# Optimization experiments

Hardware: AMD Instinct MI355X
Metric: run time of the kernel (lower is better)

## Reference

```python
import jax, jax.numpy as jnp
import numpy as np

ITERATIONS = 20  # Resonator(iterations=20)
B, F, V, D = 128, 4, 2048, 4096


def _hardsign(x):
    # bipolar normalization used by MAP-VSA multiset(normalize=True); ties -> +1
    return jnp.where(x >= 0, 1.0, -1.0).astype(x.dtype)


def setup_inputs() -> dict:
    key = jax.random.key(0)
    k1, k2 = jax.random.split(key, 2)
    # bipolar codebooks: (F, V, D)
    codebooks = _hardsign(jax.random.normal(k1, (F, V, D), dtype=jnp.float32))
    # a realistic composite input: bind (elementwise product) of one codevector per factor
    idx = jax.random.randint(k2, (B, F), 0, V)                       # (B, F)
    chosen = codebooks[jnp.arange(F)[None, :], idx]                  # (B, F, D)
    inputs = jnp.prod(chosen, axis=1)                                # (B, D)
    # standard resonator init: normalized superposition of each codebook
    init_estimates = jnp.broadcast_to(
        _hardsign(jnp.sum(codebooks, axis=1)), (B, F, D)
    ).astype(jnp.float32)                                            # (B, F, D)
    return {"inputs": inputs, "init_estimates": init_estimates, "codebooks": codebooks}


def _resonator_step(inputs, est, codebooks):
    # est: (B, F, D). rolled stack over k=1..F-1 -> (B, F, F-1, D)
    f = est.shape[-2]
    rolled = jnp.stack([jnp.roll(est, k, axis=-2) for k in range(1, f)], axis=-2)
    inv_others = jnp.prod(rolled, axis=-2)          # multibind over dim -2 -> (B, F, D)
    new_est = inputs[:, None, :] * inv_others       # bind -> (B, F, D)
    sim = jnp.einsum('bfd,fvd->bfv', new_est, codebooks)   # similarity (activation='NONE')
    # multiset(codebooks, sim, normalize=True)
    return _hardsign(jnp.einsum('bfv,fvd->bfd', sim, codebooks))


def reference(inputs, init_estimates, codebooks):
    def body(carry, i):
        est, k, done = carry
        new = _resonator_step(inputs, est, codebooks)
        eq = jnp.all(new == est)          # convergence check (fixed point)
        k = jnp.where(done, k, i)
        return (new, k, done | eq), None

    carry0 = (init_estimates, jnp.int32(0), jnp.bool_(False))
    (est, k, _), _ = jax.lax.scan(body, carry0, jnp.arange(ITERATIONS, dtype=jnp.int32))
    # cleanup: argmax of |similarity| per factor (argmax_abs=True)
    sim = jnp.einsum('bfd,fvd->bfv', est, codebooks)
    outcome = jnp.argmax(jnp.abs(sim), axis=-1)     # (B, F) int indices
    return outcome, k
```

## Files before the change

kernel.cpp:

```cpp
#include <hip/hip_runtime.h>
#include <hip/hip_bf16.h>
#include <stdint.h>

#define B_    128
#define F_    4
#define V_    2048
#define D_    4096
#define DW    64
#define VW    32
#define ITERS 20
#define NKT   16

typedef _Float16 half8 __attribute__((ext_vector_type(8)));
typedef float   floatx4 __attribute__((ext_vector_type(4)));

__global__ __launch_bounds__(256) void k_pack(const float* __restrict__ x,
                                              uint64_t* __restrict__ bits, int n) {
    int t = blockIdx.x * blockDim.x + threadIdx.x;
    if (t * 16 >= n) return;
    const float4* p = (const float4*)x + (size_t)t * 4;
    uint32_t m = 0;
    #pragma unroll
    for (int j = 0; j < 4; ++j) {
        float4 v = p[j];
        m |= (__float_as_uint(v.x) >> 31) << (4 * j + 0);
        m |= (__float_as_uint(v.y) >> 31) << (4 * j + 1);
        m |= (__float_as_uint(v.z) >> 31) << (4 * j + 2);
        m |= (__float_as_uint(v.w) >> 31) << (4 * j + 3);
    }
    ((unsigned short*)bits)[t] = (unsigned short)m;
}

__global__ void k_packT(const uint64_t* __restrict__ cb_bits,
                        uint64_t* __restrict__ cbT) {
    int vw = blockIdx.x, dwg = blockIdx.y, f = blockIdx.z;
    int lane = threadIdx.x & 63;
    int dw = dwg * 4 + (threadIdx.x >> 6);
    uint64_t w = cb_bits[((size_t)f * V_ + vw * 64 + lane) * DW + dw];
    uint64_t r = 0;
    for (int d2 = 0; d2 < 64; ++d2) {
        uint64_t m = __ballot((unsigned)((w >> d2) & 1));
        if (lane == d2) r = m;
    }
    cbT[((size_t)f * D_ + dw * 64 + lane) * VW + vw] = r;
}

__global__ __launch_bounds__(256) void k_sim(
        const uint64_t* __restrict__ cb_bits,
        const uint64_t* __restrict__ in_bits,
        const uint64_t* __restrict__ est_bits,
        _Float16* __restrict__ simf,
        const int* __restrict__ flags, int iter) {
    if (iter > 0 && flags[iter - 1] == 0) return;
    int vt = blockIdx.x, bt = blockIdx.y, f = blockIdx.z;
    int v0 = vt * 64, b0 = bt * 64;
    int tid = threadIdx.x;

    __shared__ __align__(16) ulonglong2 CB2[64 * 32];
    __shared__ __align__(16) ulonglong2 NB2[64 * 32];

    #pragma unroll
    for (int it = 0; it < 8; ++it) {
        int cq = it * 256 + tid;
        int r = cq >> 5, ch = cq & 31;
        const ulonglong2* src = (const ulonglong2*)(cb_bits + ((size_t)f * V_ + v0 + r) * DW);
        CB2[r * 32 + (ch ^ (r & 7))] = src[ch];
    }
    #pragma unroll
    for (int it = 0; it < 8; ++it) {
        int cq = it * 256 + tid;
        int r = cq >> 5, ch = cq & 31;
        int b = b0 + r;
        const ulonglong2* iv = (const ulonglong2*)(in_bits + (size_t)b * DW);
        const uint64_t* eb = est_bits + (size_t)b * F_ * DW;
        ulonglong2 i2 = iv[ch];
        ulonglong2 e0 = ((const ulonglong2*)(eb + 0 * DW))[ch];
        ulonglong2 e1 = ((const ulonglong2*)(eb + 1 * DW))[ch];
        ulonglong2 e2 = ((const ulonglong2*)(eb + 2 * DW))[ch];
        ulonglong2 e3 = ((const ulonglong2*)(eb + 3 * DW))[ch];
        ulonglong2 es = e0;
        if (f == 1) es = e1; else if (f == 2) es = e2; else if (f == 3) es = e3;
        ulonglong2 val;
        val.x = i2.x ^ e0.x ^ e1.x ^ e2.x ^ e3.x ^ es.x;
        val.y = i2.y ^ e0.y ^ e1.y ^ e2.y ^ e3.y ^ es.y;
        NB2[r * 32 + (ch ^ (r & 7))] = val;
    }
    __syncthreads();

    int vv = tid & 15, bb = tid >> 4;
    int svz = vv & 7, sbz = bb & 7;
    int pc[4][4];
    #pragma unroll
    for (int j = 0; j < 4; ++j)
        #pragma unroll
        for (int i = 0; i < 4; ++i) pc[j][i] = 0;

    #pragma unroll 4
    for (int ch = 0; ch < 32; ++ch) {
        ulonglong2 c[4], n[4];
        #pragma unroll
        for (int i = 0; i < 4; ++i)
            c[i] = CB2[(vv + 16 * i) * 32 + (ch ^ svz)];
        #pragma unroll
        for (int j = 0; j < 4; ++j)
            n[j] = NB2[(bb + 16 * j) * 32 + (ch ^ sbz)];
        #pragma unroll
        for (int j = 0; j < 4; ++j)
            #pragma unroll
            for (int i = 0; i < 4; ++i)
                pc[j][i] += __popcll(n[j].x ^ c[i].x) + __popcll(n[j].y ^ c[i].y);
    }

    #pragma unroll
    for (int j = 0; j < 4; ++j) {
        int b = b0 + bb + 16 * j;
        #pragma unroll
        for (int i = 0; i < 4; ++i) {
            int v = v0 + vv + 16 * i;
            simf[((size_t)f * B_ + b) * V_ + v] = (_Float16)(2048 - pc[j][i]);
        }
    }
}

__global__ __launch_bounds__(256) void k_gemm(
        const _Float16* __restrict__ simf,
        const uint64_t* __restrict__ cbT,
        uint64_t* __restrict__ est_bits,
        int* __restrict__ flags, int iter) {
    if (iter > 0 && flags[iter - 1] == 0) return;
    int nt = blockIdx.x, mt = blockIdx.y, f = blockIdx.z;
    int m0 = mt * 64, n0 = nt * 64;
    int tid = threadIdx.x;
    int lane = tid & 63, wave = tid >> 6;
    int lrow = lane & 15, lq = lane >> 4;
    int wm = wave & 1, wn = wave >> 1;

    __shared__ __align__(16) uint64_t Bb[64 * VW];
    __shared__ __align__(16) _Float16 As[64 * 128];
    __shared__ int bd;
    if (tid == 0) bd = 0;

    const uint64_t* bsrc = cbT + ((size_t)f * D_ + n0) * VW;
    #pragma unroll
    for (int p = 0; p < 4; ++p) {
        int chunk = p * 256 + tid;
        int dloc = chunk >> 4, cw = chunk & 15;
        ulonglong2 val = *(const ulonglong2*)&bsrc[dloc * VW + cw * 2];
        *(ulonglong2*)&Bb[dloc * VW + ((cw ^ (dloc & 15)) * 2)] = val;
    }

    const _Float16* Ab = simf + (size_t)f * B_ * V_ + (size_t)m0 * V_;
    int arow = tid >> 4, acol = tid & 15;
    half8 areg[4];
    #pragma unroll
    for (int p = 0; p < 4; ++p)
        areg[p] = *(const half8*)&Ab[(size_t)(p * 16 + arow) * V_ + acol * 8];

    floatx4 acc[2][2] = {};

    const uint64_t SPREAD = 0x1000200040008000ull;
    const uint64_t SMASK  = 0x8000800080008000ull;
    const uint64_t PONE   = 0x3C003C003C003C00ull;

    #pragma unroll 1
    for (int kt = 0; kt < NKT; ++kt) {
        __syncthreads();
        #pragma unroll
        for (int p = 0; p < 4; ++p)
            *(half8*)&As[(p * 16 + arow) * 128 + ((acol ^ arow) * 8)] = areg[p];
        if (kt + 1 < NKT) {
            #pragma unroll
            for (int p = 0; p < 4; ++p)
                areg[p] = *(const half8*)&Ab[(size_t)(p * 16 + arow) * V_ + (kt + 1) * 128 + acol * 8];
        }
        __syncthreads();

        ulonglong2 bw[2];
        #pragma unroll
        for (int nt2 = 0; nt2 < 2; ++nt2) {
            int dloc = wn * 32 + nt2 * 16 + lrow;
            bw[nt2] = *(const ulonglong2*)&Bb[dloc * VW + ((kt ^ (dloc & 15)) * 2)];
        }
        #pragma unroll
        for (int ks = 0; ks < 4; ++ks) {
            half8 af[2];
            #pragma unroll
            for (int mt2 = 0; mt2 < 2; ++mt2) {
                int row = wm * 32 + mt2 * 16 + lrow;
                af[mt2] = *(const half8*)&As[row * 128 + (((ks * 4 + lq) ^ lrow) * 8)];
            }
            half8 bfrag[2];
            #pragma unroll
            for (int nt2 = 0; nt2 < 2; ++nt2) {
                uint64_t w = (ks < 2) ? bw[nt2].x : bw[nt2].y;
                uint32_t byte = (uint32_t)(w >> ((((ks & 1) * 4 + lq)) * 8)) & 0xFFu;
                union { uint64_t q[2]; half8 h; } bu;
                bu.q[0] = (((uint64_t)(byte & 0xFu) * SPREAD) & SMASK) ^ PONE;
                bu.q[1] = (((uint64_t)(byte >> 4)   * SPREAD) & SMASK) ^ PONE;
                bfrag[nt2] = bu.h;
            }
            #pragma unroll
            for (int mt2 = 0; mt2 < 2; ++mt2)
                #pragma unroll
                for (int nt2 = 0; nt2 < 2; ++nt2)
                    acc[mt2][nt2] = __builtin_amdgcn_mfma_f32_16x16x32_f16(
                        af[mt2], bfrag[nt2], acc[mt2][nt2], 0, 0, 0);
        }
    }

    __syncthreads();
    unsigned char* S = (unsigned char*)As;
    #pragma unroll
    for (int mt2 = 0; mt2 < 2; ++mt2)
        #pragma unroll
        for (int nt2 = 0; nt2 < 2; ++nt2)
            #pragma unroll
            for (int r = 0; r < 4; ++r) {
                int row = wm * 32 + mt2 * 16 + lq * 4 + r;
                int col = wn * 32 + nt2 * 16 + lrow;
                S[row * 64 + col] = (acc[mt2][nt2][r] < 0.0f) ? 1 : 0;
            }
    __syncthreads();
    if (tid < 64) {
        const uint64_t* Sw = (const uint64_t*)S;
        uint64_t m = 0;
        #pragma unroll
        for (int j = 0; j < 8; ++j) {
            uint64_t w = Sw[tid * 8 + j];
            m |= ((w * 0x0102040810204080ull) >> 56) << (8 * j);
        }
        size_t widx = ((size_t)(m0 + tid) * F_ + f) * DW + nt;
        uint64_t old = est_bits[widx];
        est_bits[widx] = m;
        if (old != m) atomicOr(&bd, 1);
    }
    __syncthreads();
    if (tid == 0 && bd) atomicOr(&flags[iter], 1);
}

__global__ __launch_bounds__(256) void k_argmax(
        const uint64_t* __restrict__ cb_bits,
        const uint64_t* __restrict__ est_bits,
        int* __restrict__ keys) {
    int vt = blockIdx.x, f = blockIdx.y;
    int v0 = vt * 32;
    int tid = threadIdx.x;

    __shared__ __align__(16) ulonglong2 EB2[128 * 32];
    __shared__ __align__(16) ulonglong2 CBa[32 * 32];

    #pragma unroll
    for (int it = 0; it < 16; ++it) {
        int cq = it * 256 + tid;
        int r = cq >> 5, ch = cq & 31;
        const ulonglong2* src = (const ulonglong2*)(est_bits + ((size_t)r * F_ + f) * DW);
        EB2[r * 32 + (ch ^ (r & 7))] = src[ch];
    }
    #pragma unroll
    for (int it = 0; it < 4; ++it) {
        int cq = it * 256 + tid;
        int r = cq >> 5, ch = cq & 31;
        const ulonglong2* src = (const ulonglong2*)(cb_bits + ((size_t)f * V_ + v0 + r) * DW);
        CBa[r * 32 + (ch ^ (r & 7))] = src[ch];
    }
    __syncthreads();

    int vv = tid & 15, bb = tid >> 4;
    int svz = vv & 7, sbz = bb & 7;
    int pc[8][2];
    #pragma unroll
    for (int j = 0; j < 8; ++j) { pc[j][0] = 0; pc[j][1] = 0; }

    #pragma unroll 4
    for (int ch = 0; ch < 32; ++ch) {
        ulonglong2 c[2], n[8];
        #pragma unroll
        for (int i = 0; i < 2; ++i)
            c[i] = CBa[(vv + 16 * i) * 32 + (ch ^ svz)];
        #pragma unroll
        for (int j = 0; j < 8; ++j)
            n[j] = EB2[(bb + 16 * j) * 32 + (ch ^ sbz)];
        #pragma unroll
        for (int j = 0; j < 8; ++j)
            #pragma unroll
            for (int i = 0; i < 2; ++i)
                pc[j][i] += __popcll(n[j].x ^ c[i].x) + __popcll(n[j].y ^ c[i].y);
    }

    #pragma unroll
    for (int j = 0; j < 8; ++j) {
        int kj = 0x80000000;
        #pragma unroll
        for (int i = 0; i < 2; ++i) {
            int v = v0 + vv + 16 * i;
            int m = 2048 - pc[j][i]; if (m < 0) m = -m;
            int key = (m << 11) | (2047 - v);
            if (key > kj) kj = key;
        }
        #pragma unroll
        for (int s = 1; s < 16; s <<= 1) {
            int o = __shfl_xor(kj, s, 64);
            if (o > kj) kj = o;
        }
        if ((tid & 15) == 0)
            atomicMax(&keys[(size_t)(bb + 16 * j) * F_ + f], kj);
    }
}

__global__ void k_final(const int* __restrict__ keys, const int* __restrict__ flags,
                        int* __restrict__ out) {
    int tid = blockIdx.x * blockDim.x + threadIdx.x;
    if (tid < B_ * F_) out[tid] = 2047 - (keys[tid] & 0x7FF);
    if (tid == 0) {
        int k = ITERS - 1;
        for (int i = 0; i < ITERS; ++i) if (flags[i] == 0) { k = i; break; }
        out[B_ * F_] = k;
    }
}

extern "C" void kernel_launch(void* const* d_in, const int* in_sizes, int n_in,
                              void* d_out, int out_size, void* d_ws, size_t ws_size,
                              hipStream_t stream) {
    const float* inputs = (const float*)d_in[0];
    const float* inite  = (const float*)d_in[1];
    const float* cb     = (const float*)d_in[2];
    int* out = (int*)d_out;

    char* ws = (char*)d_ws;
    uint64_t* cb_bits  = (uint64_t*)ws;  ws += (size_t)F_ * V_ * DW * 8;
    uint64_t* cbT_bits = (uint64_t*)ws;  ws += (size_t)F_ * D_ * VW * 8;
    uint64_t* est_bits = (uint64_t*)ws;  ws += (size_t)B_ * F_ * DW * 8;
    uint64_t* in_bits  = (uint64_t*)ws;  ws += (size_t)B_ * DW * 8;
    _Float16* simf     = (_Float16*)ws;  ws += (size_t)F_ * B_ * V_ * 2;
    int*      flags    = (int*)ws;       ws += 32 * 4;
    int*      keys     = (int*)ws;       ws += B_ * F_ * 4;

    hipMemsetAsync(flags, 0, (32 + B_ * F_) * sizeof(int), stream);
    k_pack<<<(F_ * V_ * D_) / 4096, 256, 0, stream>>>(cb,     cb_bits,  F_ * V_ * D_);
    k_pack<<<(B_ * F_ * D_) / 4096, 256, 0, stream>>>(inite,  est_bits, B_ * F_ * D_);
    k_pack<<<(B_ * D_) / 4096,      256, 0, stream>>>(inputs, in_bits,  B_ * D_);
    k_packT<<<dim3(32, 16, 4), 256, 0, stream>>>(cb_bits, cbT_bits);

    for (int i = 0; i < ITERS; ++i) {
        k_sim<<<dim3(32, 2, 4), 256, 0, stream>>>(cb_bits, in_bits, est_bits, simf, flags, i);
        k_gemm<<<dim3(64, 2, 4), 256, 0, stream>>>(simf, cbT_bits, est_bits, flags, i);
    }
    k_argmax<<<dim3(64, 4), 256, 0, stream>>>(cb_bits, est_bits, keys);
    k_final<<<2, 256, 0, stream>>>(keys, flags, out);
}
```

Before: 1.005 ms.

## Fuse setup packing and memset into one kernel; halve k_sim batch tile

Merges the three bit-packing launches and the flags/keys memset into a single k_setup kernel. This cuts launch overhead and the memset call. It also halves k_sim's batch tile from 64 to 32 rows, doubling the grid to 512 blocks for better occupancy on the many CUs, at the cost of reloading the codebook tile twice as often. The per-factor estimate select becomes an indexed load.

```diff
diff --git a/kernel.cpp b/kernel.cpp
--- a/kernel.cpp
+++ b/kernel.cpp
@@ -1,5 +1,4 @@
 #include <hip/hip_runtime.h>
-#include <hip/hip_bf16.h>
 #include <stdint.h>
 
 #define B_    128
@@ -14,10 +13,8 @@
 typedef _Float16 half8 __attribute__((ext_vector_type(8)));
 typedef float   floatx4 __attribute__((ext_vector_type(4)));
 
-__global__ __launch_bounds__(256) void k_pack(const float* __restrict__ x,
-                                              uint64_t* __restrict__ bits, int n) {
-    int t = blockIdx.x * blockDim.x + threadIdx.x;
-    if (t * 16 >= n) return;
+__device__ __forceinline__ void pack16(const float* __restrict__ x,
+                                       uint64_t* __restrict__ bits, int t) {
     const float4* p = (const float4*)x + (size_t)t * 4;
     uint32_t m = 0;
     #pragma unroll
@@ -29,6 +26,22 @@
         m |= (__float_as_uint(v.w) >> 31) << (4 * j + 3);
     }
     ((unsigned short*)bits)[t] = (unsigned short)m;
+}
+
+__global__ __launch_bounds__(256) void k_setup(
+        const float* __restrict__ cb, const float* __restrict__ inite,
+        const float* __restrict__ inputs,
+        uint64_t* __restrict__ cb_bits, uint64_t* __restrict__ est_bits,
+        uint64_t* __restrict__ in_bits,
+        int* __restrict__ flags, int* __restrict__ keys) {
+    int gtid = blockIdx.x * 256 + threadIdx.x;
+    const int T = 512 * 256;
+    const int ncb = (F_ * V_ * D_) / 16;
+    for (int t = gtid; t < ncb; t += T) pack16(cb, cb_bits, t);
+    pack16(inite, est_bits, gtid);
+    if (gtid < (B_ * D_) / 16) pack16(inputs, in_bits, gtid);
+    if (gtid < 32) flags[gtid] = 0;
+    if (gtid < B_ * F_) keys[gtid] = 0;
 }
 
 __global__ void k_packT(const uint64_t* __restrict__ cb_bits,
@@ -53,11 +66,11 @@
         const int* __restrict__ flags, int iter) {
     if (iter > 0 && flags[iter - 1] == 0) return;
     int vt = blockIdx.x, bt = blockIdx.y, f = blockIdx.z;
-    int v0 = vt * 64, b0 = bt * 64;
+    int v0 = vt * 64, b0 = bt * 32;
     int tid = threadIdx.x;
 
     __shared__ __align__(16) ulonglong2 CB2[64 * 32];
-    __shared__ __align__(16) ulonglong2 NB2[64 * 32];
+    __shared__ __align__(16) ulonglong2 NB2[32 * 32];
 
     #pragma unroll
     for (int it = 0; it < 8; ++it) {
@@ -67,7 +80,7 @@
         CB2[r * 32 + (ch ^ (r & 7))] = src[ch];
     }
     #pragma unroll
-    for (int it = 0; it < 8; ++it) {
+    for (int it = 0; it < 4; ++it) {
         int cq = it * 256 + tid;
         int r = cq >> 5, ch = cq & 31;
         int b = b0 + r;
@@ -78,8 +91,7 @@
         ulonglong2 e1 = ((const ulonglong2*)(eb + 1 * DW))[ch];
         ulonglong2 e2 = ((const ulonglong2*)(eb + 2 * DW))[ch];
         ulonglong2 e3 = ((const ulonglong2*)(eb + 3 * DW))[ch];
-        ulonglong2 es = e0;
-        if (f == 1) es = e1; else if (f == 2) es = e2; else if (f == 3) es = e3;
+        ulonglong2 es = ((const ulonglong2*)(eb + (size_t)f * DW))[ch];
         ulonglong2 val;
         val.x = i2.x ^ e0.x ^ e1.x ^ e2.x ^ e3.x ^ es.x;
         val.y = i2.y ^ e0.y ^ e1.y ^ e2.y ^ e3.y ^ es.y;
@@ -89,30 +101,29 @@
 
     int vv = tid & 15, bb = tid >> 4;
     int svz = vv & 7, sbz = bb & 7;
-    int pc[4][4];
-    #pragma unroll
-    for (int j = 0; j < 4; ++j)
+    int pc[2][4];
+    #pragma unroll
+    for (int j = 0; j < 2; ++j)
         #pragma unroll
         for (int i = 0; i < 4; ++i) pc[j][i] = 0;
 
     #pragma unroll 4
     for (int ch = 0; ch < 32; ++ch) {
-        ulonglong2 c[4], n[4];
+        ulonglong2 c[4], n[2];
         #pragma unroll
         for (int i = 0; i < 4; ++i)
             c[i] = CB2[(vv + 16 * i) * 32 + (ch ^ svz)];
         #pragma unroll
-        for (int j = 0; j < 4; ++j)
+        for (int j = 0; j < 2; ++j)
             n[j] = NB2[(bb + 16 * j) * 32 + (ch ^ sbz)];
         #pragma unroll
-        for (int j = 0; j < 4; ++j)
+        for (int j = 0; j < 2; ++j)
             #pragma unroll
             for (int i = 0; i < 4; ++i)
                 pc[j][i] += __popcll(n[j].x ^ c[i].x) + __popcll(n[j].y ^ c[i].y);
     }
-
-    #pragma unroll
-    for (int j = 0; j < 4; ++j) {
+    #pragma unroll
+    for (int j = 0; j < 2; ++j) {
         int b = b0 + bb + 16 * j;
         #pragma unroll
         for (int i = 0; i < 4; ++i) {
@@ -289,7 +300,7 @@
 
     #pragma unroll
     for (int j = 0; j < 8; ++j) {
-        int kj = 0x80000000;
+        int kj = (int)0x80000000;
         #pragma unroll
         for (int i = 0; i < 2; ++i) {
             int v = v0 + vv + 16 * i;
@@ -335,14 +346,12 @@
     int*      flags    = (int*)ws;       ws += 32 * 4;
     int*      keys     = (int*)ws;       ws += B_ * F_ * 4;
 
-    hipMemsetAsync(flags, 0, (32 + B_ * F_) * sizeof(int), stream);
-    k_pack<<<(F_ * V_ * D_) / 4096, 256, 0, stream>>>(cb,     cb_bits,  F_ * V_ * D_);
-    k_pack<<<(B_ * F_ * D_) / 4096, 256, 0, stream>>>(inite,  est_bits, B_ * F_ * D_);
-    k_pack<<<(B_ * D_) / 4096,      256, 0, stream>>>(inputs, in_bits,  B_ * D_);
+    k_setup<<<512, 256, 0, stream>>>(cb, inite, inputs, cb_bits, est_bits,
+                                     in_bits, flags, keys);
     k_packT<<<dim3(32, 16, 4), 256, 0, stream>>>(cb_bits, cbT_bits);
 
     for (int i = 0; i < ITERS; ++i) {
-        k_sim<<<dim3(32, 2, 4), 256, 0, stream>>>(cb_bits, in_bits, est_bits, simf, flags, i);
+        k_sim<<<dim3(32, 4, 4), 256, 0, stream>>>(cb_bits, in_bits, est_bits, simf, flags, i);
         k_gemm<<<dim3(64, 2, 4), 256, 0, stream>>>(simf, cbT_bits, est_bits, flags, i);
     }
     k_argmax<<<dim3(64, 4), 256, 0, stream>>>(cb_bits, est_bits, keys);
```

Measured after the change: 950.4 us. 5.4% less time.
